# Optimization experiments

Hardware: AMD Instinct MI355X
Metric: run time of the kernel (lower is better)

Reference implementation:

```python
import jax, jax.numpy as jnp
import numpy as np

TOP_K = 8
NUM_GROUPS = 8


def setup_inputs() -> dict:
    key = jax.random.key(0)
    ks = jax.random.split(key, 6)
    T_B, T_S, H, I, E, G = 1, 2048, 2048, 768, 32, NUM_GROUPS
    hidden_states = jax.random.normal(ks[0], (T_B, T_S, H), dtype=jnp.float32)
    gate_weight = jax.random.normal(ks[1], (E, H), dtype=jnp.float32) * 0.02
    gate_up_proj = jax.random.normal(ks[2], (E, 2 * I, H), dtype=jnp.float32) * 0.02
    down_proj = jax.random.normal(ks[3], (E, H, I), dtype=jnp.float32) * 0.02
    merge_groups = jax.random.randint(ks[4], (E,), 0, G, dtype=jnp.int64)
    # ensure every group id appears at least once so dominant experts are well-defined
    merge_groups = merge_groups.at[:G].set(jnp.arange(G, dtype=jnp.int64))
    dominant_experts = jax.random.randint(ks[5], (G,), 0, E, dtype=jnp.int64)
    return {
        "hidden_states": hidden_states,
        "gate_weight": gate_weight,
        "gate_up_proj": gate_up_proj,
        "down_proj": down_proj,
        "merge_groups": merge_groups,
        "dominant_experts": dominant_experts,
    }


def reference(hidden_states, gate_weight, gate_up_proj, down_proj, merge_groups, dominant_experts):
    B, S, H = hidden_states.shape
    G = dominant_experts.shape[0]
    x = hidden_states.reshape(-1, H)  # [T, H]

    # Router: softmax over all experts, then top-k of the probabilities (as in source)
    logits = jnp.einsum("th,eh->te", x, gate_weight)
    probs = jax.nn.softmax(logits.astype(jnp.float32), axis=-1).astype(logits.dtype)
    top_val, top_idx = jax.lax.top_k(probs, TOP_K)  # [T, K]
    top_val = top_val / jnp.sum(top_val, axis=-1, keepdims=True)  # norm_topk_prob

    # Each selected expert e is replaced by its group's dominant expert; by linearity
    # of the scatter-add combine, sum routing weights per (token, group).
    sel_group = merge_groups[top_idx]  # [T, K] in [0, G)
    onehot = jax.nn.one_hot(sel_group, G, dtype=top_val.dtype)  # [T, K, G]
    w_tg = jnp.einsum("tk,tkg->tg", top_val, onehot)  # combined weight per token/group

    gu = gate_up_proj[dominant_experts]  # [G, 2I, H]
    dn = down_proj[dominant_experts]     # [G, H, I]

    h = jnp.einsum("th,goh->tgo", x, gu)           # [T, G, 2I]
    gate, up = jnp.split(h, 2, axis=-1)              # [T, G, I] each
    act = jax.nn.silu(gate) * up                     # SwiGLU
    y = jnp.einsum("tgi,ghi->tgh", act, dn)        # [T, G, H]
    out = jnp.einsum("tg,tgh->th", w_tg, y)        # combine
    return out.reshape(B, S, H)
```

## Files before the change

### kernel.cpp

```cpp
#include <hip/hip_runtime.h>
#include <hip/hip_bf16.h>

typedef __attribute__((ext_vector_type(8))) short short8v;
typedef __attribute__((ext_vector_type(4))) float f32x4;

#define T_TOK 2048
#define HDIM  2048
#define IDIM  768
#define NGRP  8

__device__ __forceinline__ unsigned short f2b(float f){
  unsigned u = __float_as_uint(f);
  u = u + 0x7FFFu + ((u >> 16) & 1u);
  return (unsigned short)(u >> 16);
}
__device__ __forceinline__ float b2f(unsigned short s){
  return __uint_as_float(((unsigned)s) << 16);
}

__global__ __launch_bounds__(256) void router_kernel(
    const float* __restrict__ x, const float* __restrict__ gw,
    const int* __restrict__ mg, float* __restrict__ wtg,
    unsigned short* __restrict__ xb)
{
  __shared__ float xs[4][2048];
  __shared__ float lg[4][32];
  int tid = threadIdx.x;
  int t0 = blockIdx.x * 4;

  #pragma unroll
  for (int k = 0; k < 8; k++){
    int idx = k*256 + tid;
    int tok = idx >> 9, wi = idx & 511;
    float4 v = ((const float4*)(x + (size_t)(t0 + tok)*HDIM))[wi];
    ((float4*)xs[tok])[wi] = v;
    ushort4 b; b.x=f2b(v.x); b.y=f2b(v.y); b.z=f2b(v.z); b.w=f2b(v.w);
    ((ushort4*)(xb + (size_t)(t0+tok)*HDIM))[wi] = b;
  }
  __syncthreads();

  int e = tid >> 3, ch = tid & 7;
  float s0=0.f, s1=0.f, s2=0.f, s3=0.f;
  const float4* gv = (const float4*)(gw + (size_t)e*HDIM);
  #pragma unroll 4
  for (int k = 0; k < 64; k++){
    int i4 = ch + 8*k;
    float4 b  = gv[i4];
    float4 a0 = ((const float4*)xs[0])[i4];
    float4 a1 = ((const float4*)xs[1])[i4];
    float4 a2 = ((const float4*)xs[2])[i4];
    float4 a3 = ((const float4*)xs[3])[i4];
    s0 += a0.x*b.x + a0.y*b.y + a0.z*b.z + a0.w*b.w;
    s1 += a1.x*b.x + a1.y*b.y + a1.z*b.z + a1.w*b.w;
    s2 += a2.x*b.x + a2.y*b.y + a2.z*b.z + a2.w*b.w;
    s3 += a3.x*b.x + a3.y*b.y + a3.z*b.z + a3.w*b.w;
  }
  #pragma unroll
  for (int off=1; off<8; off<<=1){
    s0 += __shfl_xor(s0, off); s1 += __shfl_xor(s1, off);
    s2 += __shfl_xor(s2, off); s3 += __shfl_xor(s3, off);
  }
  if (ch == 0){ lg[0][e]=s0; lg[1][e]=s1; lg[2][e]=s2; lg[3][e]=s3; }
  __syncthreads();

  int wv = tid >> 6, lane = tid & 63;
  float val = (lane < 32) ? lg[wv][lane] : -1e30f;
  float mx = val;
  #pragma unroll
  for (int off=16; off; off>>=1) mx = fmaxf(mx, __shfl_xor(mx, off));
  float p = (lane < 32) ? expf(val - mx) : 0.f;
  float sm = p;
  #pragma unroll
  for (int off=16; off; off>>=1) sm += __shfl_xor(sm, off);
  float v = (lane < 32) ? (p / sm) : -1.f;
  int idx = lane;
  float vals[8]; int idxs[8];
  #pragma unroll
  for (int it=0; it<8; it++){
    float bv = v; int bi = idx;
    #pragma unroll
    for (int off=32; off; off>>=1){
      float ov = __shfl_xor(bv, off); int oi = __shfl_xor(bi, off);
      if (ov > bv || (ov == bv && oi < bi)){ bv = ov; bi = oi; }
    }
    vals[it] = bv; idxs[it] = bi;
    if (lane == bi) v = -1.f;
  }
  float tot = vals[0]+vals[1]+vals[2]+vals[3]+vals[4]+vals[5]+vals[6]+vals[7];
  float racc = 0.f;
  #pragma unroll
  for (int it=0; it<8; it++){
    int grp = mg[idxs[it]];
    if (lane == grp) racc += vals[it] / tot;
  }
  if (lane < 8) wtg[(size_t)(t0+wv)*NGRP + lane] = racc;
}

__global__ __launch_bounds__(256) void convert_gu_kernel(
    const float* __restrict__ src, unsigned short* __restrict__ dst,
    const int* __restrict__ de)
{
  int g = blockIdx.z;
  int i4 = blockIdx.x*256 + threadIdx.x;
  int j  = i4 >> 9;
  int c4 = i4 & 511;
  int q = j >> 5, r = j & 31;
  int srow = (r < 16) ? (q*16 + r) : (768 + q*16 + (r - 16));
  const float4* s = (const float4*)(src + ((size_t)de[g]*1536 + srow)*HDIM);
  float4 vv = s[c4];
  ushort4 b; b.x=f2b(vv.x); b.y=f2b(vv.y); b.z=f2b(vv.z); b.w=f2b(vv.w);
  ((ushort4*)(dst + ((size_t)g*1536 + j)*HDIM))[c4] = b;
}

__global__ __launch_bounds__(256) void convert_dn_kernel(
    const float* __restrict__ src, unsigned short* __restrict__ dst,
    const int* __restrict__ de)
{
  int g = blockIdx.z;
  size_t i4 = (size_t)blockIdx.x*256 + threadIdx.x;
  const float4* s = (const float4*)(src + (size_t)de[g]*1572864);
  float4 vv = s[i4];
  ushort4 b; b.x=f2b(vv.x); b.y=f2b(vv.y); b.z=f2b(vv.z); b.w=f2b(vv.w);
  ((ushort4*)(dst + (size_t)g*1572864))[i4] = b;
}


template<int R>
__device__ __forceinline__ void stage512(const unsigned short* __restrict__ gsrc,
                                         int ldE, unsigned short* __restrict__ lds,
                                         int tid)
{
  #pragma unroll
  for (int j = 0; j < R/128; j++){
    int row = j*128 + (tid >> 2);
    const unsigned short* src = gsrc + (size_t)row*ldE + (tid & 3)*8;
    __builtin_amdgcn_global_load_lds(
        (const __attribute__((address_space(1))) void*)src,
        (__attribute__((address_space(3))) void*)(lds + j*4096 + (tid >> 6)*512),
        16, 0, 0);
  }
}

template<int R>
__device__ __forceinline__ void stage256(const unsigned short* __restrict__ gsrc,
                                         int ldE, unsigned short* __restrict__ lds,
                                         int tid)
{
  #pragma unroll
  for (int j = 0; j < R/64; j++){
    int row = j*64 + (tid >> 2);
    const unsigned short* src = gsrc + (size_t)row*ldE + (tid & 3)*8;
    __builtin_amdgcn_global_load_lds(
        (const __attribute__((address_space(1))) void*)src,
        (__attribute__((address_space(3))) void*)(lds + j*2048 + (tid >> 6)*512),
        16, 0, 0);
  }
}

__device__ __forceinline__ short8v rfrag(const unsigned short* lds, int r, int s){
  return *(const short8v*)((const char*)lds + r*64 + (s << 4));
}

#define WAITV(N)  asm volatile("s_waitcnt vmcnt(" #N ")" ::: "memory")
#define TOPBAR()  do { __builtin_amdgcn_s_barrier(); __builtin_amdgcn_sched_barrier(0); } while(0)
#define PIN()     do { asm volatile("s_waitcnt lgkmcnt(0)" ::: "memory"); __builtin_amdgcn_sched_barrier(0); } while(0)

__global__ __launch_bounds__(256, 2) void gemm1_kernel(
    const unsigned short* __restrict__ xb, const unsigned short* __restrict__ gu,
    const float* __restrict__ wtg, unsigned short* __restrict__ actb)
{
  __shared__ unsigned short Al[3][8192];
  __shared__ unsigned short Bl[3][4096];
  int tid = threadIdx.x, lane = tid & 63, w = tid >> 6;
  int wm = w >> 1, wn = w & 1;
  int fr = lane & 15, sl = lane >> 4;

  int bid = blockIdx.x;
  int xcd = bid & 7, j = bid >> 3;
  int panel = ((xcd & 1) ? 48 : 0) + (j >> 1);
  int mb = ((xcd >> 1) << 1) + (j & 1);
  int nb = panel % 12, g = panel / 12;
  int m0 = mb * 256, n0 = nb * 128;
  const unsigned short* Abase = xb + (size_t)m0 * HDIM;
  const unsigned short* Bbase = gu + ((size_t)g * 1536 + n0) * HDIM;

  f32x4 acc[8][4];
  #pragma unroll
  for (int m=0;m<8;m++){
    #pragma unroll
    for (int n=0;n<4;n++) acc[m][n] = (f32x4){0,0,0,0};
  }

  #define BODY1(t, CB, SB, DOSTAGE) do { \
    const unsigned short* Ab = &Al[CB][0]; \
    const unsigned short* Bb = &Bl[CB][0]; \
    short8v av[8], bv[4]; \
    _Pragma("unroll") for (int m=0;m<8;m++) av[m] = rfrag(Ab, wm*128 + m*16 + fr, sl); \
    _Pragma("unroll") for (int n=0;n<4;n++) bv[n] = rfrag(Bb, wn*64 + n*16 + fr, sl); \
    if (DOSTAGE){ int k2 = (t)+2; \
      stage256<256>(Abase + k2*32, HDIM, &Al[SB][0], tid); \
      stage256<128>(Bbase + k2*32, HDIM, &Bl[SB][0], tid); } \
    PIN(); \
    __builtin_amdgcn_s_setprio(1); \
    _Pragma("unroll") for (int m=0;m<8;m++){ \
      _Pragma("unroll") for (int n=0;n<4;n++){ \
        acc[m][n] = __builtin_amdgcn_mfma_f32_16x16x32_bf16(av[m], bv[n], acc[m][n],0,0,0); } } \
    __builtin_amdgcn_s_setprio(0); \
  } while(0)

  const int NT = 64;
  stage256<256>(Abase,      HDIM, &Al[0][0], tid);
  stage256<128>(Bbase,      HDIM, &Bl[0][0], tid);
  stage256<256>(Abase + 32, HDIM, &Al[1][0], tid);
  stage256<128>(Bbase + 32, HDIM, &Bl[1][0], tid);

  int cb = 0, sb = 2;
  for (int t = 0; t < NT-2; ++t){
    WAITV(6); TOPBAR();
    BODY1(t, cb, sb, 1);
    cb = (cb==2)?0:cb+1; sb = (sb==2)?0:sb+1;
  }
  WAITV(6); TOPBAR(); BODY1(NT-2, cb, sb, 0);
  cb = (cb==2)?0:cb+1;
  WAITV(0); TOPBAR(); BODY1(NT-1, cb, sb, 0);
  #undef BODY1

  int r0 = (lane >> 4) * 4;
  int q0 = (n0 + wn*64) >> 5;
  #pragma unroll
  for (int m = 0; m < 8; m++){
    int trow = m0 + wm*128 + m*16 + r0;
    #pragma unroll
    for (int q = 0; q < 2; q++){
      int icol = (q0 + q)*16 + fr;
      #pragma unroll
      for (int jj = 0; jj < 4; jj++){
        int t = trow + jj;
        float wv = wtg[(size_t)t*NGRP + g];
        float gf = acc[m][2*q][jj];
        float uf = acc[m][2*q+1][jj];
        float sg = gf / (1.f + expf(-gf));
        actb[((size_t)g*T_TOK + t)*IDIM + icol] = f2b(sg * uf * wv);
      }
    }
  }
}

__global__ __launch_bounds__(512, 2) void gemm2_kernel(
    const unsigned short* __restrict__ actb, const unsigned short* __restrict__ dnb,
    float* __restrict__ part)
{
  __shared__ unsigned short Al[3][8192];
  __shared__ unsigned short Bl[3][8192];
  int tid = threadIdx.x, lane = tid & 63, w = tid >> 6;
  int wm = w >> 2, wn = w & 3;
  int fr = lane & 15, sl = lane >> 4;

  int bid = blockIdx.x;
  int xcd = bid & 7, j = bid >> 3;
  int panel = ((xcd & 1) ? 16 : 0) + (j >> 1);
  int mb = ((xcd >> 1) << 1) + (j & 1);
  int nb = panel & 7, z = panel >> 3;
  int m0 = mb * 256, n0 = nb * 256;

  f32x4 acc[8][4];
  #pragma unroll
  for (int m=0;m<8;m++){
    #pragma unroll
    for (int n=0;n<4;n++) acc[m][n] = (f32x4){0,0,0,0};
  }

  #define STAGE2(kt, SB) do { \
    int gi = (kt) / 24; int kk = ((kt) - gi*24) * 32; int gg = z*2 + gi; \
    stage512<256>(actb + ((size_t)gg*T_TOK + m0)*IDIM + kk, IDIM, &Al[SB][0], tid); \
    stage512<256>(dnb  + ((size_t)gg*HDIM + n0)*IDIM + kk, IDIM, &Bl[SB][0], tid); \
  } while(0)

  #define BODY2(t, CB, SB, DOSTAGE) do { \
    const unsigned short* Ab = &Al[CB][0]; \
    const unsigned short* Bb = &Bl[CB][0]; \
    short8v av[8], bv[4]; \
    _Pragma("unroll") for (int m=0;m<8;m++) av[m] = rfrag(Ab, wm*128 + m*16 + fr, sl); \
    _Pragma("unroll") for (int n=0;n<4;n++) bv[n] = rfrag(Bb, wn*64 + n*16 + fr, sl); \
    if (DOSTAGE){ STAGE2((t)+2, SB); } \
    PIN(); \
    __builtin_amdgcn_s_setprio(1); \
    _Pragma("unroll") for (int m=0;m<8;m++){ \
      _Pragma("unroll") for (int n=0;n<4;n++){ \
        acc[m][n] = __builtin_amdgcn_mfma_f32_16x16x32_bf16(av[m], bv[n], acc[m][n],0,0,0); } } \
    __builtin_amdgcn_s_setprio(0); \
  } while(0)

  const int NT = 48;
  STAGE2(0, 0); STAGE2(1, 1);

  int cb = 0, sb = 2;
  for (int t = 0; t < NT-2; ++t){
    WAITV(4); TOPBAR();
    BODY2(t, cb, sb, 1);
    cb = (cb==2)?0:cb+1; sb = (sb==2)?0:sb+1;
  }
  WAITV(4); TOPBAR(); BODY2(NT-2, cb, sb, 0);
  cb = (cb==2)?0:cb+1;
  WAITV(0); TOPBAR(); BODY2(NT-1, cb, sb, 0);
  #undef BODY2
  #undef STAGE2

  float* Cb = part + (size_t)z * T_TOK * HDIM;
  int r0 = (lane >> 4) * 4;
  #pragma unroll
  for (int m = 0; m < 8; m++){
    int row = m0 + wm*128 + m*16 + r0;
    #pragma unroll
    for (int n = 0; n < 4; n++){
      int cc = n0 + wn*64 + n*16 + fr;
      #pragma unroll
      for (int jj = 0; jj < 4; jj++){
        Cb[(size_t)(row + jj)*HDIM + cc] = acc[m][n][jj];
      }
    }
  }
}

__global__ __launch_bounds__(256) void reduce_kernel(
    const float* __restrict__ p, float* __restrict__ o)
{
  size_t i = ((size_t)blockIdx.x*256 + threadIdx.x)*4;
  float4 a0 = *(const float4*)(p + i);
  float4 a1 = *(const float4*)(p + 4194304 + i);
  float4 a2 = *(const float4*)(p + 8388608 + i);
  float4 a3 = *(const float4*)(p + 12582912 + i);
  float4 r;
  r.x = a0.x + a1.x + a2.x + a3.x;
  r.y = a0.y + a1.y + a2.y + a3.y;
  r.z = a0.z + a1.z + a2.z + a3.z;
  r.w = a0.w + a1.w + a2.w + a3.w;
  *(float4*)(o + i) = r;
}

extern "C" void kernel_launch(void* const* d_in, const int* in_sizes, int n_in,
                              void* d_out, int out_size, void* d_ws, size_t ws_size,
                              hipStream_t stream)
{
  (void)in_sizes; (void)n_in; (void)out_size; (void)ws_size;
  const float* x   = (const float*)d_in[0];
  const float* gw  = (const float*)d_in[1];
  const float* gup = (const float*)d_in[2];
  const float* dnp = (const float*)d_in[3];
  const int*   mg  = (const int*)d_in[4];
  const int*   de  = (const int*)d_in[5];
  float* out = (float*)d_out;
  char* ws = (char*)d_ws;

  float*          wtg  = (float*)(ws + 0);
  unsigned short* xb   = (unsigned short*)(ws + 65536);
  unsigned short* dnb  = (unsigned short*)(ws + 8454144);
  unsigned short* actb = (unsigned short*)(ws + 33619968);
  unsigned short* gub  = (unsigned short*)(ws + 58785792);
  float*          part = (float*)(ws + 58785792);

  router_kernel<<<512, 256, 0, stream>>>(x, gw, mg, wtg, xb);
  convert_gu_kernel<<<dim3(3072,1,8), 256, 0, stream>>>(gup, gub, de);
  convert_dn_kernel<<<dim3(1536,1,8), 256, 0, stream>>>(dnp, dnb, de);
  gemm1_kernel<<<768, 256, 0, stream>>>(xb, gub, wtg, actb);
  gemm2_kernel<<<256, 512, 0, stream>>>(actb, dnb, part);
  reduce_kernel<<<4096, 256, 0, stream>>>(part, out);
}
```

Before: 243.9 us.

## Retile gemm2 to 128x256 with 2-way split-K and merge convert kernels

Result: no change. 243.5 us (-0.1%).

```diff
diff --git a/kernel.cpp b/kernel.cpp
--- a/kernel.cpp
+++ b/kernel.cpp
@@ -96,34 +96,48 @@
   if (lane < 8) wtg[(size_t)(t0+wv)*NGRP + lane] = racc;
 }
 
-__global__ __launch_bounds__(256) void convert_gu_kernel(
-    const float* __restrict__ src, unsigned short* __restrict__ dst,
+__global__ __launch_bounds__(256) void convert_kernel(
+    const float* __restrict__ gup, const float* __restrict__ dnp,
+    unsigned short* __restrict__ gub, unsigned short* __restrict__ dnb,
     const int* __restrict__ de)
 {
   int g = blockIdx.z;
-  int i4 = blockIdx.x*256 + threadIdx.x;
-  int j  = i4 >> 9;
-  int c4 = i4 & 511;
-  int q = j >> 5, r = j & 31;
-  int srow = (r < 16) ? (q*16 + r) : (768 + q*16 + (r - 16));
-  const float4* s = (const float4*)(src + ((size_t)de[g]*1536 + srow)*HDIM);
-  float4 vv = s[c4];
-  ushort4 b; b.x=f2b(vv.x); b.y=f2b(vv.y); b.z=f2b(vv.z); b.w=f2b(vv.w);
-  ((ushort4*)(dst + ((size_t)g*1536 + j)*HDIM))[c4] = b;
-}
-
-__global__ __launch_bounds__(256) void convert_dn_kernel(
-    const float* __restrict__ src, unsigned short* __restrict__ dst,
-    const int* __restrict__ de)
-{
-  int g = blockIdx.z;
-  size_t i4 = (size_t)blockIdx.x*256 + threadIdx.x;
-  const float4* s = (const float4*)(src + (size_t)de[g]*1572864);
-  float4 vv = s[i4];
-  ushort4 b; b.x=f2b(vv.x); b.y=f2b(vv.y); b.z=f2b(vv.z); b.w=f2b(vv.w);
-  ((ushort4*)(dst + (size_t)g*1572864))[i4] = b;
-}
-
+  int bx = blockIdx.x;
+  if (bx < 3072){
+    int i4 = bx*256 + threadIdx.x;
+    int j  = i4 >> 9;
+    int c4 = i4 & 511;
+    int q = j >> 5, r = j & 31;
+    int srow = (r < 16) ? (q*16 + r) : (768 + q*16 + (r - 16));
+    const float4* s = (const float4*)(gup + ((size_t)de[g]*1536 + srow)*HDIM);
+    float4 vv = s[c4];
+    ushort4 b; b.x=f2b(vv.x); b.y=f2b(vv.y); b.z=f2b(vv.z); b.w=f2b(vv.w);
+    ((ushort4*)(gub + ((size_t)g*1536 + j)*HDIM))[c4] = b;
+  } else {
+    size_t i4 = (size_t)(bx - 3072)*256 + threadIdx.x;
+    const float4* s = (const float4*)(dnp + (size_t)de[g]*1572864);
+    float4 vv = s[i4];
+    ushort4 b; b.x=f2b(vv.x); b.y=f2b(vv.y); b.z=f2b(vv.z); b.w=f2b(vv.w);
+    ((ushort4*)(dnb + (size_t)g*1572864))[i4] = b;
+  }
+}
+
+
+template<int R>
+__device__ __forceinline__ void stage256(const unsigned short* __restrict__ gsrc,
+                                         int ldE, unsigned short* __restrict__ lds,
+                                         int tid)
+{
+  #pragma unroll
+  for (int j = 0; j < R/64; j++){
+    int row = j*64 + (tid >> 2);
+    const unsigned short* src = gsrc + (size_t)row*ldE + (tid & 3)*8;
+    __builtin_amdgcn_global_load_lds(
+        (const __attribute__((address_space(1))) void*)src,
+        (__attribute__((address_space(3))) void*)(lds + j*2048 + (tid >> 6)*512),
+        16, 0, 0);
+  }
+}
 
 template<int R>
 __device__ __forceinline__ void stage512(const unsigned short* __restrict__ gsrc,
@@ -137,22 +151,6 @@
     __builtin_amdgcn_global_load_lds(
         (const __attribute__((address_space(1))) void*)src,
         (__attribute__((address_space(3))) void*)(lds + j*4096 + (tid >> 6)*512),
-        16, 0, 0);
-  }
-}
-
-template<int R>
-__device__ __forceinline__ void stage256(const unsigned short* __restrict__ gsrc,
-                                         int ldE, unsigned short* __restrict__ lds,
-                                         int tid)
-{
-  #pragma unroll
-  for (int j = 0; j < R/64; j++){
-    int row = j*64 + (tid >> 2);
-    const unsigned short* src = gsrc + (size_t)row*ldE + (tid & 3)*8;
-    __builtin_amdgcn_global_load_lds(
-        (const __attribute__((address_space(1))) void*)src,
-        (__attribute__((address_space(3))) void*)(lds + j*2048 + (tid >> 6)*512),
         16, 0, 0);
   }
 }
@@ -246,11 +244,11 @@
   }
 }
 
-__global__ __launch_bounds__(512, 2) void gemm2_kernel(
+__global__ __launch_bounds__(512, 4) void gemm2_kernel(
     const unsigned short* __restrict__ actb, const unsigned short* __restrict__ dnb,
     float* __restrict__ part)
 {
-  __shared__ unsigned short Al[3][8192];
+  __shared__ unsigned short Al[3][4096];
   __shared__ unsigned short Bl[3][8192];
   int tid = threadIdx.x, lane = tid & 63, w = tid >> 6;
   int wm = w >> 2, wn = w & 3;
@@ -258,49 +256,47 @@
 
   int bid = blockIdx.x;
   int xcd = bid & 7, j = bid >> 3;
-  int panel = ((xcd & 1) ? 16 : 0) + (j >> 1);
-  int mb = ((xcd >> 1) << 1) + (j & 1);
+  int panel = ((xcd & 1) ? 8 : 0) + (j >> 2);
+  int mb = ((xcd >> 1) << 2) + (j & 3);
   int nb = panel & 7, z = panel >> 3;
-  int m0 = mb * 256, n0 = nb * 256;
-
-  f32x4 acc[8][4];
-  #pragma unroll
-  for (int m=0;m<8;m++){
+  int m0 = mb * 128, n0 = nb * 256;
+
+  f32x4 acc[4][4];
+  #pragma unroll
+  for (int m=0;m<4;m++){
     #pragma unroll
     for (int n=0;n<4;n++) acc[m][n] = (f32x4){0,0,0,0};
   }
 
-  #define STAGE2(kt, SB) do { \
-    int gi = (kt) / 24; int kk = ((kt) - gi*24) * 32; int gg = z*2 + gi; \
-    stage512<256>(actb + ((size_t)gg*T_TOK + m0)*IDIM + kk, IDIM, &Al[SB][0], tid); \
-    stage512<256>(dnb  + ((size_t)gg*HDIM + n0)*IDIM + kk, IDIM, &Bl[SB][0], tid); \
+  #define STAGE2(kt, b2) do { \
+    int gi = (kt) / 24; int kk = ((kt) - gi*24) * 32; int gg = z*4 + gi; \
+    stage512<128>(actb + ((size_t)gg*T_TOK + m0)*IDIM + kk, IDIM, &Al[b2][0], tid); \
+    stage512<256>(dnb  + ((size_t)gg*HDIM + n0)*IDIM + kk, IDIM, &Bl[b2][0], tid); \
   } while(0)
 
   #define BODY2(t, CB, SB, DOSTAGE) do { \
-    const unsigned short* Ab = &Al[CB][0]; \
-    const unsigned short* Bb = &Bl[CB][0]; \
-    short8v av[8], bv[4]; \
-    _Pragma("unroll") for (int m=0;m<8;m++) av[m] = rfrag(Ab, wm*128 + m*16 + fr, sl); \
-    _Pragma("unroll") for (int n=0;n<4;n++) bv[n] = rfrag(Bb, wn*64 + n*16 + fr, sl); \
+    short8v av[4], bv[4]; \
+    _Pragma("unroll") for (int m=0;m<4;m++) av[m] = rfrag(&Al[CB][0], wm*64 + m*16 + fr, sl); \
+    _Pragma("unroll") for (int n=0;n<4;n++) bv[n] = rfrag(&Bl[CB][0], wn*64 + n*16 + fr, sl); \
     if (DOSTAGE){ STAGE2((t)+2, SB); } \
     PIN(); \
     __builtin_amdgcn_s_setprio(1); \
-    _Pragma("unroll") for (int m=0;m<8;m++){ \
+    _Pragma("unroll") for (int m=0;m<4;m++){ \
       _Pragma("unroll") for (int n=0;n<4;n++){ \
         acc[m][n] = __builtin_amdgcn_mfma_f32_16x16x32_bf16(av[m], bv[n], acc[m][n],0,0,0); } } \
     __builtin_amdgcn_s_setprio(0); \
   } while(0)
 
-  const int NT = 48;
+  const int NT = 96;
   STAGE2(0, 0); STAGE2(1, 1);
 
   int cb = 0, sb = 2;
   for (int t = 0; t < NT-2; ++t){
-    WAITV(4); TOPBAR();
+    WAITV(3); TOPBAR();
     BODY2(t, cb, sb, 1);
     cb = (cb==2)?0:cb+1; sb = (sb==2)?0:sb+1;
   }
-  WAITV(4); TOPBAR(); BODY2(NT-2, cb, sb, 0);
+  WAITV(3); TOPBAR(); BODY2(NT-2, cb, sb, 0);
   cb = (cb==2)?0:cb+1;
   WAITV(0); TOPBAR(); BODY2(NT-1, cb, sb, 0);
   #undef BODY2
@@ -309,8 +305,8 @@
   float* Cb = part + (size_t)z * T_TOK * HDIM;
   int r0 = (lane >> 4) * 4;
   #pragma unroll
-  for (int m = 0; m < 8; m++){
-    int row = m0 + wm*128 + m*16 + r0;
+  for (int m = 0; m < 4; m++){
+    int row = m0 + wm*64 + m*16 + r0;
     #pragma unroll
     for (int n = 0; n < 4; n++){
       int cc = n0 + wn*64 + n*16 + fr;
@@ -328,13 +324,11 @@
   size_t i = ((size_t)blockIdx.x*256 + threadIdx.x)*4;
   float4 a0 = *(const float4*)(p + i);
   float4 a1 = *(const float4*)(p + 4194304 + i);
-  float4 a2 = *(const float4*)(p + 8388608 + i);
-  float4 a3 = *(const float4*)(p + 12582912 + i);
   float4 r;
-  r.x = a0.x + a1.x + a2.x + a3.x;
-  r.y = a0.y + a1.y + a2.y + a3.y;
-  r.z = a0.z + a1.z + a2.z + a3.z;
-  r.w = a0.w + a1.w + a2.w + a3.w;
+  r.x = a0.x + a1.x;
+  r.y = a0.y + a1.y;
+  r.z = a0.z + a1.z;
+  r.w = a0.w + a1.w;
   *(float4*)(o + i) = r;
 }
 
@@ -360,8 +354,7 @@
   float*          part = (float*)(ws + 58785792);
 
   router_kernel<<<512, 256, 0, stream>>>(x, gw, mg, wtg, xb);
-  convert_gu_kernel<<<dim3(3072,1,8), 256, 0, stream>>>(gup, gub, de);
-  convert_dn_kernel<<<dim3(1536,1,8), 256, 0, stream>>>(dnp, dnb, de);
+  convert_kernel<<<dim3(4608,1,8), 256, 0, stream>>>(gup, dnp, gub, dnb, de);
   gemm1_kernel<<<768, 256, 0, stream>>>(xb, gub, wtg, actb);
   gemm2_kernel<<<256, 512, 0, stream>>>(actb, dnb, part);
   reduce_kernel<<<4096, 256, 0, stream>>>(part, out);
```
